# Kernel tuning notes

Measured on AMD Instinct MI355X. Metric: run time of the kernel, lower is better.

## Reference

```python
import jax, jax.numpy as jnp
import numpy as np

K = 3  # neighbor_count


def setup_inputs() -> dict:
    key = jax.random.key(0)
    k1, k2, k3, k4, k5 = jax.random.split(key, 5)
    N, M, D = 200000, 64, 256
    node_features = jax.random.normal(k1, (N, D), dtype=jnp.float32)
    neighbors = jax.random.randint(k2, (N, M), 0, N, dtype=jnp.int64)
    # valid neighbor counts; clamp to >= K so every node has a full top-k
    neighbor_counts = jnp.maximum(
        jax.random.randint(k3, (N,), 0, M, dtype=jnp.int64), K)
    W = jax.random.normal(k4, (2 * D,), dtype=jnp.float32) * 0.05
    b = jax.random.normal(k5, (1,), dtype=jnp.float32) * 0.05
    return {"node_features": node_features, "neighbors": neighbors,
            "neighbor_counts": neighbor_counts, "W": W, "b": b}


def reference(node_features, neighbors, neighbor_counts, W, b):
    # fc([x_i ; x_j]) = x_i . W[:D] + x_j . W[D:] + b  (Linear(2D, 1))
    D = node_features.shape[1]
    wa, wb = W[:D], W[D:]
    s_self = node_features @ wa + b[0]          # [N]
    s_all = node_features @ wb                  # [N]
    s_nb = s_all[neighbors]                     # [N, M] gather
    scores = jnp.exp(jax.nn.leaky_relu(s_self[:, None] + s_nb))  # [N, M]
    valid = jnp.arange(neighbors.shape[1])[None, :] < neighbor_counts[:, None]
    scores = jnp.where(valid, scores, -jnp.inf)
    top_vals, top_idx = jax.lax.top_k(scores, K)              # [N, K]
    selected = jnp.take_along_axis(neighbors, top_idx, axis=1)  # [N, K] node ids
    return top_vals, selected
```

## Files before the change

### kernel.cpp

```cpp
#include <hip/hip_runtime.h>
#include <cstdint>

#define D_DIM 256
#define M_DIM 64
#define K_TOP 3

__global__ __launch_bounds__(256) void ns_scores_kernel(
    const float* __restrict__ nf,
    const float* __restrict__ W,
    const float* __restrict__ b,
    float* __restrict__ s_self,
    float* __restrict__ s_all,
    int N)
{
    const int gtid = blockIdx.x * blockDim.x + threadIdx.x;
    const int row  = gtid >> 6;
    const int lane = threadIdx.x & 63;
    if (row >= N) return;

    const float4 v  = ((const float4*)(nf + (size_t)row * D_DIM))[lane];
    const float4 wa = ((const float4*)W)[lane];
    const float4 wb = ((const float4*)(W + D_DIM))[lane];

    float sa = v.x * wa.x + v.y * wa.y + v.z * wa.z + v.w * wa.w;
    float sb = v.x * wb.x + v.y * wb.y + v.z * wb.z + v.w * wb.w;

    #pragma unroll
    for (int off = 32; off > 0; off >>= 1) {
        sa += __shfl_down(sa, off);
        sb += __shfl_down(sb, off);
    }
    if (lane == 0) {
        s_self[row] = sa + b[0];
        s_all[row]  = sb;
    }
}

__global__ __launch_bounds__(256) void ns_topk_kernel(
    const int* __restrict__ neighbors,
    const int* __restrict__ counts,
    const float* __restrict__ s_self,
    const float* __restrict__ s_all,
    float* __restrict__ out_vals,
    float* __restrict__ out_idx,
    int N)
{
    const int gtid = blockIdx.x * blockDim.x + threadIdx.x;
    const int row  = gtid >> 6;
    const int lane = threadIdx.x & 63;
    if (row >= N) return;

    const int nbr = neighbors[(size_t)row * M_DIM + lane];
    const int cnt = counts[row];
    const float ss = s_self[row];

    float score = 0.0f;
    if (lane < cnt) {
        const float x  = ss + s_all[nbr];
        const float lr = (x >= 0.0f) ? x : 0.01f * x;
        score = expf(lr);
    }

    unsigned long long key =
        ((unsigned long long)__float_as_uint(score) << 32) |
        (unsigned long long)(63 - lane);

    float vals[K_TOP];
    int   idxs[K_TOP];

    #pragma unroll
    for (int k = 0; k < K_TOP; ++k) {
        unsigned long long m = key;
        #pragma unroll
        for (int off = 32; off > 0; off >>= 1) {
            const unsigned long long o = __shfl_xor(m, off);
            if (o > m) m = o;
        }
        const int jwin = 63 - (int)(m & 0xFFFFFFFFull);
        vals[k] = __uint_as_float((unsigned)(m >> 32));
        idxs[k] = __shfl(nbr, jwin);
        if (lane == jwin) {
            key = (unsigned long long)(63 - lane);
        }
    }

    if (lane == 0) {
        const size_t base = (size_t)row * K_TOP;
        #pragma unroll
        for (int k = 0; k < K_TOP; ++k) {
            out_vals[base + k] = vals[k];
            out_idx [base + k] = (float)idxs[k];
        }
    }
}

extern "C" void kernel_launch(void* const* d_in, const int* in_sizes, int n_in,
                              void* d_out, int out_size, void* d_ws, size_t ws_size,
                              hipStream_t stream)
{
    const float* nf        = (const float*)d_in[0];
    const int*   neighbors = (const int*)  d_in[1];
    const int*   counts    = (const int*)  d_in[2];
    const float* W         = (const float*)d_in[3];
    const float* b         = (const float*)d_in[4];

    const int N = in_sizes[2];

    float* s_self = (float*)d_ws;
    float* s_all  = s_self + N;

    float* out_vals = (float*)d_out;
    float* out_idx  = out_vals + (size_t)N * K_TOP;

    const int threads = 256;
    const int wavesPerBlock = threads / 64;
    const int blocks = (N + wavesPerBlock - 1) / wavesPerBlock;

    ns_scores_kernel<<<blocks, threads, 0, stream>>>(nf, W, b, s_self, s_all, N);
    ns_topk_kernel<<<blocks, threads, 0, stream>>>(neighbors, counts, s_self, s_all,
                                                   out_vals, out_idx, N);
}
```

Measured before the change: 370.1 us.

## Process four rows per wavefront with 16-lane subgroups in both kernels

Both kernels now map four rows per 64-lane wavefront, with each 16-lane subgroup handling one row. The scores kernel loops over four float4 chunks per lane and reduces over 16 lanes. The top-k kernel loads int4 neighbor vectors and takes a local max over four keys before a 4-step shuffle reduction. The aim is to cut shuffle steps and per-row overhead and to widen loads, at the cost of more per-thread work and more registers.

```diff
diff --git a/kernel.cpp b/kernel.cpp
--- a/kernel.cpp
+++ b/kernel.cpp
@@ -4,6 +4,8 @@
 #define D_DIM 256
 #define M_DIM 64
 #define K_TOP 3
+
+typedef unsigned long long u64;
 
 __global__ __launch_bounds__(256) void ns_scores_kernel(
     const float* __restrict__ nf,
@@ -13,24 +15,34 @@
     float* __restrict__ s_all,
     int N)
 {
-    const int gtid = blockIdx.x * blockDim.x + threadIdx.x;
-    const int row  = gtid >> 6;
+    const int wave = (blockIdx.x * blockDim.x + threadIdx.x) >> 6;
     const int lane = threadIdx.x & 63;
+    const int sub  = lane >> 4;
+    const int p    = lane & 15;
+    const int row  = wave * 4 + sub;
     if (row >= N) return;
 
-    const float4 v  = ((const float4*)(nf + (size_t)row * D_DIM))[lane];
-    const float4 wa = ((const float4*)W)[lane];
-    const float4 wb = ((const float4*)(W + D_DIM))[lane];
+    const float4* __restrict__ vrow = (const float4*)(nf + (size_t)row * D_DIM);
+    const float4* __restrict__ wa4  = (const float4*)W;
+    const float4* __restrict__ wb4  = (const float4*)(W + D_DIM);
 
-    float sa = v.x * wa.x + v.y * wa.y + v.z * wa.z + v.w * wa.w;
-    float sb = v.x * wb.x + v.y * wb.y + v.z * wb.z + v.w * wb.w;
+    float sa = 0.0f, sb = 0.0f;
+    #pragma unroll
+    for (int i = 0; i < 4; ++i) {
+        const int o = i * 16 + p;
+        const float4 v = vrow[o];
+        const float4 a = wa4[o];
+        const float4 c = wb4[o];
+        sa += v.x * a.x + v.y * a.y + v.z * a.z + v.w * a.w;
+        sb += v.x * c.x + v.y * c.y + v.z * c.z + v.w * c.w;
+    }
 
     #pragma unroll
-    for (int off = 32; off > 0; off >>= 1) {
-        sa += __shfl_down(sa, off);
-        sb += __shfl_down(sb, off);
+    for (int off = 8; off > 0; off >>= 1) {
+        sa += __shfl_xor(sa, off);
+        sb += __shfl_xor(sb, off);
     }
-    if (lane == 0) {
+    if (p == 0) {
         s_self[row] = sa + b[0];
         s_all[row]  = sb;
     }
@@ -45,46 +57,64 @@
     float* __restrict__ out_idx,
     int N)
 {
-    const int gtid = blockIdx.x * blockDim.x + threadIdx.x;
-    const int row  = gtid >> 6;
+    const int wave = (blockIdx.x * blockDim.x + threadIdx.x) >> 6;
     const int lane = threadIdx.x & 63;
+    const int sub  = lane >> 4;
+    const int p    = lane & 15;
+    const int row  = wave * 4 + sub;
     if (row >= N) return;
 
-    const int nbr = neighbors[(size_t)row * M_DIM + lane];
-    const int cnt = counts[row];
+    const int4 nb = ((const int4*)(neighbors + (size_t)row * M_DIM))[p];
+    const int  cnt = counts[row];
     const float ss = s_self[row];
 
-    float score = 0.0f;
-    if (lane < cnt) {
-        const float x  = ss + s_all[nbr];
-        const float lr = (x >= 0.0f) ? x : 0.01f * x;
-        score = expf(lr);
+    const int nbs[4] = { nb.x, nb.y, nb.z, nb.w };
+    u64 key[4];
+    #pragma unroll
+    for (int e = 0; e < 4; ++e) {
+        const int j = p * 4 + e;
+        float score = 0.0f;
+        if (j < cnt) {
+            const float x  = ss + s_all[nbs[e]];
+            const float lr = (x >= 0.0f) ? x : 0.01f * x;
+            score = expf(lr);
+        }
+        key[e] = ((u64)__float_as_uint(score) << 32) | (u64)(63 - j);
     }
-
-    unsigned long long key =
-        ((unsigned long long)__float_as_uint(score) << 32) |
-        (unsigned long long)(63 - lane);
 
     float vals[K_TOP];
     int   idxs[K_TOP];
 
     #pragma unroll
     for (int k = 0; k < K_TOP; ++k) {
-        unsigned long long m = key;
+        u64 m = key[0];
+        if (key[1] > m) m = key[1];
+        if (key[2] > m) m = key[2];
+        if (key[3] > m) m = key[3];
         #pragma unroll
-        for (int off = 32; off > 0; off >>= 1) {
-            const unsigned long long o = __shfl_xor(m, off);
+        for (int off = 8; off > 0; off >>= 1) {
+            const u64 o = __shfl_xor(m, off);
             if (o > m) m = o;
         }
-        const int jwin = 63 - (int)(m & 0xFFFFFFFFull);
+        const int jwin = 63 - (int)(m & 0x3F);
         vals[k] = __uint_as_float((unsigned)(m >> 32));
-        idxs[k] = __shfl(nbr, jwin);
-        if (lane == jwin) {
-            key = (unsigned long long)(63 - lane);
+
+        const int ew = jwin & 3;
+        const int pw = jwin >> 2;
+        const int cand = (ew == 0) ? nbs[0] : (ew == 1) ? nbs[1]
+                       : (ew == 2) ? nbs[2] : nbs[3];
+        idxs[k] = __shfl(cand, (sub << 4) | pw);
+
+        if (p == pw) {
+            const u64 dead = (u64)(63 - jwin);
+            if      (ew == 0) key[0] = dead;
+            else if (ew == 1) key[1] = dead;
+            else if (ew == 2) key[2] = dead;
+            else              key[3] = dead;
         }
     }
 
-    if (lane == 0) {
+    if (p == 0) {
         const size_t base = (size_t)row * K_TOP;
         #pragma unroll
         for (int k = 0; k < K_TOP; ++k) {
@@ -113,8 +143,8 @@
     float* out_idx  = out_vals + (size_t)N * K_TOP;
 
     const int threads = 256;
-    const int wavesPerBlock = threads / 64;
-    const int blocks = (N + wavesPerBlock - 1) / wavesPerBlock;
+    const int rowsPerBlock = (threads / 64) * 4;
+    const int blocks = (N + rowsPerBlock - 1) / rowsPerBlock;
 
     ns_scores_kernel<<<blocks, threads, 0, stream>>>(nf, W, b, s_self, s_all, N);
     ns_topk_kernel<<<blocks, threads, 0, stream>>>(neighbors, counts, s_self, s_all,
```

New measurement: 339.5 us. 1.09x faster.
